# Optimization experiments

Measured on AMD Instinct MI355X. Metric: run time of the kernel, lower is better.

The kernel has to match this reference:

```python
import jax, jax.numpy as jnp
import numpy as np

G, N, DEG = 256, 128, 16          # graphs, nodes/graph, avg degree
C_IN, H, C_OUT = 128, 256, 128    # channels = [128,256,256,128]
K1, HEADS = 75, 4                 # GMT: ceil(0.25*300) seeds, 4 heads
NTOT, E = G * N, G * N * DEG
BN_EPS = 1e-5


def _bn(h, gamma, beta):
    # BatchNorm1d, training mode (biased batch stats over nodes)
    m = h.mean(0)
    v = h.var(0)
    return (h - m) * jax.lax.rsqrt(v + BN_EPS) * gamma + beta


def _gin(x, src, dst, W1, b1, g1, be1, W2, b2, g2, be2):
    # GINConv, eps=0: MLP(x + sum_{j->i} x_j); MLP = Lin-BN-ReLU-Lin-BN
    agg = x + jax.ops.segment_sum(x[src], dst, num_segments=NTOT)
    h = jax.nn.relu(_bn(agg @ W1 + b1, g1, be1))
    return _bn(h @ W2 + b2, g2, be2)


def _gcn(x, src, dst, W, b):
    # GCNConv with self-loops and symmetric normalization
    xw = x @ W
    deg = jax.ops.segment_sum(jnp.ones((E,), x.dtype), dst, num_segments=NTOT) + 1.0
    dinv = jax.lax.rsqrt(deg)
    msg = xw[src] * (dinv[src] * dinv[dst])[:, None]
    return jax.ops.segment_sum(msg, dst, num_segments=NTOT) + xw / deg[:, None] + b


def _mab(Q, Kd, Vd, Wq, bq, Wo, bo):
    # Multihead attention block of GMT (no layer_norm, no padding mask:
    # all graphs have exactly N nodes). O = Qp + MHA(Qp,K,V); out = O + relu(fc_o(O))
    Qp = Q @ Wq + bq                                   # [B, q, H]
    B, q, h = Qp.shape
    dh = h // HEADS
    sc = jnp.einsum('bqhd,bkhd->bhqk', Qp.reshape(B, q, HEADS, dh),
                    Kd.reshape(B, -1, HEADS, dh)) / jnp.sqrt(jnp.float32(h))
    A = jax.nn.softmax(sc, axis=-1)
    O = Qp + jnp.einsum('bhqk,bkhd->bqhd', A, Vd.reshape(B, -1, HEADS, dh)).reshape(B, q, h)
    return O + jax.nn.relu(O @ Wo + bo)


def _forward(x, edge_index, batch,
             g0_W1, g0_b1, g0_gamma1, g0_beta1, g0_W2, g0_b2, g0_gamma2, g0_beta2,
             g1_W1, g1_b1, g1_gamma1, g1_beta1, g1_W2, g1_b2, g1_gamma2, g1_beta2,
             lin1_W, lin1_b, S1,
             p1_Wq, p1_Wk, p1_Wv, p1_Wo, p1_bq, p1_bk, p1_bv, p1_bo,
             s2_Wq, s2_Wk, s2_Wv, s2_Wo, s2_bq, s2_bk, s2_bv, s2_bo,
             p3_Wq, p3_Wk, p3_Wv, p3_Wo, p3_bq, p3_bk, p3_bv, p3_bo,
             S3, lin2_W, lin2_b):
    src, dst = edge_index[0], edge_index[1]
    h = jax.nn.relu(_gin(x, src, dst, g0_W1, g0_b1, g0_gamma1, g0_beta1,
                         g0_W2, g0_b2, g0_gamma2, g0_beta2))
    h = jax.nn.relu(_gin(h, src, dst, g1_W1, g1_b1, g1_gamma1, g1_beta1,
                         g1_W2, g1_b2, g1_gamma2, g1_beta2))
    xl = h @ lin1_W + lin1_b                           # post-lin1 node feats [NTOT,H]
    # GMPool_G: PMA with K1 seeds, K/V from GCNConv over the graph
    Kd = _gcn(xl, src, dst, p1_Wk, p1_bk).reshape(G, N, H)
    Vd = _gcn(xl, src, dst, p1_Wv, p1_bv).reshape(G, N, H)
    Xp = _mab(jnp.broadcast_to(S1[None], (G, K1, H)), Kd, Vd, p1_Wq, p1_bq, p1_Wo, p1_bo)
    # SelfAtt: SAB
    Xp = _mab(Xp, Xp @ s2_Wk + s2_bk, Xp @ s2_Wv + s2_bv, s2_Wq, s2_bq, s2_Wo, s2_bo)
    # GMPool_I: PMA with 1 seed
    Xp = _mab(jnp.broadcast_to(S3[None], (G, 1, H)),
              Xp @ p3_Wk + p3_bk, Xp @ p3_Wv + p3_bv, p3_Wq, p3_bq, p3_Wo, p3_bo)
    return Xp[:, 0, :] @ lin2_W + lin2_b               # [G, C_OUT]


def setup_inputs() -> dict:
    key = jax.random.key(0)
    ks = iter(jax.random.split(key, 64))
    def p(shape, scale):
        return jax.random.normal(next(ks), shape, dtype=jnp.float32) * scale
    x = jax.random.normal(next(ks), (NTOT, C_IN), dtype=jnp.float32)
    src = jax.random.randint(next(ks), (G, N * DEG), 0, N, dtype=jnp.int32)
    dst = jax.random.randint(next(ks), (G, N * DEG), 0, N, dtype=jnp.int32)
    off = (jnp.arange(G, dtype=jnp.int32) * N)[:, None]
    edge_index = jnp.stack([(src + off).reshape(-1), (dst + off).reshape(-1)])
    batch = jnp.repeat(jnp.arange(G, dtype=jnp.int32), N)
    inp = {'x': x, 'edge_index': edge_index, 'batch': batch}
    for i, (ci, co) in enumerate([(C_IN, H), (H, H)]):
        inp[f'g{i}_W1'] = p((ci, co), ci ** -0.5)
        inp[f'g{i}_b1'] = jnp.zeros((co,), jnp.float32)
        inp[f'g{i}_gamma1'] = jnp.ones((co,), jnp.float32)
        inp[f'g{i}_beta1'] = jnp.zeros((co,), jnp.float32)
        inp[f'g{i}_W2'] = p((co, co), co ** -0.5)
        inp[f'g{i}_b2'] = jnp.zeros((co,), jnp.float32)
        inp[f'g{i}_gamma2'] = jnp.ones((co,), jnp.float32)
        inp[f'g{i}_beta2'] = jnp.zeros((co,), jnp.float32)
    inp['lin1_W'] = p((H, H), H ** -0.5)
    inp['lin1_b'] = jnp.zeros((H,), jnp.float32)
    inp['S1'] = p((K1, H), H ** -0.5)
    for pre in ['p1', 's2', 'p3']:
        for nm in ['Wq', 'Wk', 'Wv', 'Wo']:
            inp[f'{pre}_{nm}'] = p((H, H), H ** -0.5)
        for nm in ['bq', 'bk', 'bv', 'bo']:
            inp[f'{pre}_{nm}'] = jnp.zeros((H,), jnp.float32)
    inp['S3'] = p((1, H), H ** -0.5)
    inp['lin2_W'] = p((H, C_OUT), H ** -0.5)
    inp['lin2_b'] = jnp.zeros((C_OUT,), jnp.float32)
    return inp


def reference(x, edge_index, batch,
              g0_W1, g0_b1, g0_gamma1, g0_beta1, g0_W2, g0_b2, g0_gamma2, g0_beta2,
              g1_W1, g1_b1, g1_gamma1, g1_beta1, g1_W2, g1_b2, g1_gamma2, g1_beta2,
              lin1_W, lin1_b, S1,
              p1_Wq, p1_Wk, p1_Wv, p1_Wo, p1_bq, p1_bk, p1_bv, p1_bo,
              s2_Wq, s2_Wk, s2_Wv, s2_Wo, s2_bq, s2_bk, s2_bv, s2_bo,
              p3_Wq, p3_Wk, p3_Wv, p3_Wo, p3_bq, p3_bk, p3_bv, p3_bo,
              S3, lin2_W, lin2_b):
    return _forward(x, edge_index, batch,
                    g0_W1, g0_b1, g0_gamma1, g0_beta1, g0_W2, g0_b2, g0_gamma2, g0_beta2,
                    g1_W1, g1_b1, g1_gamma1, g1_beta1, g1_W2, g1_b2, g1_gamma2, g1_beta2,
                    lin1_W, lin1_b, S1,
                    p1_Wq, p1_Wk, p1_Wv, p1_Wo, p1_bq, p1_bk, p1_bv, p1_bo,
                    s2_Wq, s2_Wk, s2_Wv, s2_Wo, s2_bq, s2_bk, s2_bv, s2_bo,
                    p3_Wq, p3_Wk, p3_Wv, p3_Wo, p3_bq, p3_bk, p3_bv, p3_bo,
                    S3, lin2_W, lin2_b)
```

## Files before the change

### kernel.cpp

```cpp
#include <hip/hip_runtime.h>
#include <math.h>

#define GG 256
#define NN 128
#define NTOT (GG*NN)
#define EPG 2048
#define EDGES (GG*EPG)
#define HID 256
#define DH 64

typedef __attribute__((ext_vector_type(8))) short short8;
typedef __attribute__((ext_vector_type(4))) float f32x4;

__device__ __forceinline__ ushort f2bf(float f){
  union { float f; unsigned u; } x; x.f = f;
  unsigned r = x.u + 0x7fffu + ((x.u >> 16) & 1u);
  return (ushort)(r >> 16);
}
__device__ __forceinline__ float bf2f(ushort h){
  union { unsigned u; float f; } x; x.u = ((unsigned)h) << 16;
  return x.f;
}
__device__ __forceinline__ int permR(int p){
  return ((p>>2)&3)*16 + ((p>>4)&3)*4 + (p&3) + (p&64);
}

__global__ __launch_bounds__(256) void adj_build(
    const int* __restrict__ src, const int* __restrict__ dst,
    ushort* __restrict__ adjg, float* __restrict__ dinv)
{
  __shared__ unsigned hist[NN*NN];
  int g = blockIdx.x, t = threadIdx.x;
  int base = g*EPG, nb = g*NN;
  for (int i=t; i<NN*NN; i+=256) hist[i]=0u;
  __syncthreads();
  {
    int4 a = *(const int4*)(src + base + t*8);
    int4 b = *(const int4*)(src + base + t*8 + 4);
    int4 c = *(const int4*)(dst + base + t*8);
    int4 d = *(const int4*)(dst + base + t*8 + 4);
    atomicAdd(&hist[(a.x-nb)*NN + (c.x-nb)], 1u);
    atomicAdd(&hist[(a.y-nb)*NN + (c.y-nb)], 1u);
    atomicAdd(&hist[(a.z-nb)*NN + (c.z-nb)], 1u);
    atomicAdd(&hist[(a.w-nb)*NN + (c.w-nb)], 1u);
    atomicAdd(&hist[(b.x-nb)*NN + (d.x-nb)], 1u);
    atomicAdd(&hist[(b.y-nb)*NN + (d.y-nb)], 1u);
    atomicAdd(&hist[(b.z-nb)*NN + (d.z-nb)], 1u);
    atomicAdd(&hist[(b.w-nb)*NN + (d.w-nb)], 1u);
  }
  __syncthreads();
  if (t < NN){
    unsigned dg = 0;
    for (int k=0; k<NN; k++) dg += hist[k*NN + t];
    dinv[nb + t] = rsqrtf((float)dg + 1.0f);
  }
  __syncthreads();
  ushort* out = adjg + (size_t)g*NN*NN;
  for (int idx=t; idx<NN*NN; idx+=256){
    int i = idx >> 7, kp = idx & 127;
    int j = permR(kp);
    unsigned cnt = hist[j*NN + i];
    float v = (float)cnt + ((i==j) ? 1.0f : 0.0f);
    out[idx] = f2bf(v);
  }
}

template<int MODE, int OUTBF>
__global__ __launch_bounds__(256) void agg_gemm(
    const ushort* __restrict__ adjg,
    const ushort* __restrict__ P0, const ushort* __restrict__ P1,
    const float* __restrict__ aux,
    const float* __restrict__ b0, const float* __restrict__ b1,
    void* __restrict__ out0v, void* __restrict__ out1v,
    float* __restrict__ part)
{
  const int g = blockIdx.x;
  int bn, sel = 0;
  if (MODE==2){ sel = blockIdx.y >> 1; bn = (blockIdx.y & 1)*128; }
  else bn = blockIdx.y*128;
  const ushort* Ph = (MODE==2 && sel) ? P1 : P0;
  const float* bias = (MODE==2) ? (sel ? b1 : b0) : b0;
  void* outv = (MODE==2 && sel) ? out1v : out0v;
  const int t = threadIdx.x;
  const int w = t>>6, l = t&63;
  const int wr = w>>1, wc = w&1;
  const int c16 = l&15, g16 = l>>4;
  const size_t nbase = (size_t)g*NN;
  f32x4 acc[4][4];
  #pragma unroll
  for (int i=0;i<4;i++)
    #pragma unroll
    for (int j=0;j<4;j++) acc[i][j] = (f32x4){0.f,0.f,0.f,0.f};
  const ushort* ag = adjg + (size_t)g*NN*NN;

  float sclj[4], shfj[4];
  if (MODE==1){
    #pragma unroll
    for (int j=0;j<4;j++){
      int col = bn + wc*64 + j*16 + c16;
      sclj[j] = aux[col]; shfj[j] = aux[256+col];
    }
  }

  for (int kk=0; kk<128; kk+=32){
    short8 af[4];
    #pragma unroll
    for (int i=0;i<4;i++)
      af[i] = *(const short8*)(ag + (wr*64+i*16+c16)*NN + kk + g16*8);
    short8 bh[4];
    size_t off = nbase + kk + g16*8;
    #pragma unroll
    for (int j=0;j<4;j++){
      int col = bn + wc*64 + j*16 + c16;
      short8 h8 = *(const short8*)(Ph + (size_t)col*NTOT + off);
      if (MODE==1){
        #pragma unroll
        for (int e=0;e<8;e++){
          float v = bf2f((ushort)h8[e]);
          v = fmaxf(v*sclj[j] + shfj[j], 0.f);
          h8[e] = (short)f2bf(v);
        }
      }
      bh[j] = h8;
    }
    #pragma unroll
    for (int i=0;i<4;i++)
      #pragma unroll
      for (int j=0;j<4;j++)
        acc[i][j] = __builtin_amdgcn_mfma_f32_16x16x32_bf16(af[i], bh[j], acc[i][j], 0,0,0);
  }
  float sj[4]  = {0.f,0.f,0.f,0.f};
  float s2j[4] = {0.f,0.f,0.f,0.f};
  #pragma unroll
  for (int i=0;i<4;i++){
    float4 di4 = make_float4(1.f,1.f,1.f,1.f);
    if (MODE==2) di4 = *(const float4*)(aux + nbase + wr*64 + i*16 + g16*4);
    #pragma unroll
    for (int j=0;j<4;j++){
      int col = bn + wc*64 + j*16 + c16;
      #pragma unroll
      for (int r=0;r<4;r++){
        int row = wr*64 + i*16 + g16*4 + r;
        float v = acc[i][j][r];
        if (MODE==2) v = v*(&di4.x)[r] + bias[col];
        if (MODE==3){ v = v + (bias ? bias[col] : 0.f); sj[j]+=v; s2j[j]+=v*v; }
        if (OUTBF) ((ushort*)outv)[(nbase + row)*HID + col] = f2bf(v);
        else       ((float*)outv)[(nbase + row)*HID + col] = v;
      }
    }
  }
  if (MODE==3){
    #pragma unroll
    for (int j=0;j<4;j++){
      float s = sj[j], s2 = s2j[j];
      s  += __shfl_xor(s, 16);  s  += __shfl_xor(s, 32);
      s2 += __shfl_xor(s2,16);  s2 += __shfl_xor(s2,32);
      if (g16==0){
        int col = bn + wc*64 + j*16 + c16;
        part[(g*2+wr)*256 + col]          = s;
        part[131072 + (g*2+wr)*256 + col] = s2;
      }
    }
  }
}

struct PrepW { const float* w; int K; int N; };
struct PrepArgs { PrepW e[16]; };

__global__ __launch_bounds__(256) void prep_weights(PrepArgs pa, ushort* __restrict__ wtb)
{
  __shared__ ushort T[64][72];
  int wi = blockIdx.x;
  const float* W = pa.e[wi].w;
  int K = pa.e[wi].K, N = pa.e[wi].N;
  int tk_n = K>>6, tn_n = N>>6;
  int tile = blockIdx.y;
  if (tile >= tk_n*tn_n) return;
  int tk = tile % tk_n, tn = tile / tk_n;
  int t = threadIdx.x;
  int kr = t>>2, n0 = (t&3)*16;
  #pragma unroll
  for (int j=0;j<4;j++){
    float4 v = *(const float4*)(W + (size_t)(tk*64+kr)*N + tn*64 + n0 + j*4);
    T[n0+j*4+0][kr] = f2bf(v.x);
    T[n0+j*4+1][kr] = f2bf(v.y);
    T[n0+j*4+2][kr] = f2bf(v.z);
    T[n0+j*4+3][kr] = f2bf(v.w);
  }
  __syncthreads();
  ushort* out = wtb + (size_t)wi*65536;
  int nr = t>>2, k0 = (t&3)*16;
  *(short8*)(out + (size_t)(tn*64+nr)*K + tk*64 + k0)     = *(short8*)&T[nr][k0];
  *(short8*)(out + (size_t)(tn*64+nr)*K + tk*64 + k0 + 8) = *(short8*)&T[nr][k0+8];
}

__global__ __launch_bounds__(256) void comb_bias(
    const float* __restrict__ bl, const float* __restrict__ Wk,
    const float* __restrict__ Wv, float* __restrict__ bcomb)
{
  int n = threadIdx.x;
  const float* W = blockIdx.x ? Wv : Wk;
  float s = 0.f;
  for (int k=0;k<256;k++) s += bl[k]*W[k*256+n];
  bcomb[blockIdx.x*256+n] = s;
}

__global__ __launch_bounds__(256) void bnrelu_bf(
    const ushort* __restrict__ in, const float* __restrict__ stats,
    ushort* __restrict__ outp)
{
  size_t i = ((size_t)blockIdx.x*256 + threadIdx.x)*8;
  int c = (int)(i & 255);
  short8 h = *(const short8*)(in + i);
  float4 s0 = *(const float4*)(stats + c);
  float4 s1 = *(const float4*)(stats + c + 4);
  float4 h0 = *(const float4*)(stats + 256 + c);
  float4 h1 = *(const float4*)(stats + 256 + c + 4);
  float sc[8] = {s0.x,s0.y,s0.z,s0.w,s1.x,s1.y,s1.z,s1.w};
  float sh[8] = {h0.x,h0.y,h0.z,h0.w,h1.x,h1.y,h1.z,h1.w};
  #pragma unroll
  for (int e=0;e<8;e++){
    float v = fmaxf(bf2f((ushort)h[e])*sc[e] + sh[e], 0.f);
    h[e] = (short)f2bf(v);
  }
  *(short8*)(outp + i) = h;
}

__global__ __launch_bounds__(256) void bn_final2(const float* __restrict__ part,
    const float* __restrict__ gamma, const float* __restrict__ beta, float* __restrict__ stats)
{
  int c = blockIdx.x, t = threadIdx.x;
  float s  = part[(size_t)t*256+c]          + part[(size_t)(t+256)*256+c];
  float s2 = part[131072+(size_t)t*256+c]   + part[131072+(size_t)(t+256)*256+c];
  #pragma unroll
  for (int o=1;o<64;o<<=1){ s += __shfl_xor(s,o); s2 += __shfl_xor(s2,o); }
  __shared__ float ws[8];
  int wv = t>>6;
  if ((t&63)==0){ ws[wv]=s; ws[4+wv]=s2; }
  __syncthreads();
  if (t==0){
    float S  = ws[0]+ws[1]+ws[2]+ws[3];
    float S2 = ws[4]+ws[5]+ws[6]+ws[7];
    const float invn = 1.0f/(float)NTOT;
    float mean = S*invn;
    float var  = S2*invn - mean*mean;
    float scl  = gamma[c]*rsqrtf(var + 1e-5f);
    stats[c]     = scl;
    stats[256+c] = beta[c] - mean*scl;
  }
}

template<int EPI, int ATR, int BNF, int TW, int ABF, int OBF>
__global__ __launch_bounds__(256) void mm_bf16(
    const void* __restrict__ A, const ushort* __restrict__ Wt,
    const float* __restrict__ bias, const float* __restrict__ biasB,
    const float* __restrict__ biasC, const float* __restrict__ skip,
    const float* __restrict__ bnst,
    void* __restrict__ out, ushort* __restrict__ twp,
    const float* __restrict__ rscale, float* __restrict__ part,
    int M, int K, int N)
{
  __shared__ ushort Al[64][72];
  __shared__ ushort Bl[128][72];
  const int t = threadIdx.x;
  const int bm = blockIdx.x*64, bn = blockIdx.y*128;
  const int w = t>>6, l = t&63;
  const int c16 = l&15, g16 = l>>4;
  const int ar = t>>2, ac = (t&3)*16;
  const int br = t>>1, bc = (t&1)*32;
  f32x4 acc[4][2];
  #pragma unroll
  for (int i=0;i<4;i++)
    #pragma unroll
    for (int j=0;j<2;j++) acc[i][j] = (f32x4){0.f,0.f,0.f,0.f};

  for (int k0=0; k0<K; k0+=64){
    if (ABF){
      const ushort* apb = (const ushort*)A + (size_t)(bm+ar)*K + k0 + ac;
      short8 p0 = *(const short8*)apb;
      short8 p1 = *(const short8*)(apb + 8);
      if (ATR){
        int cb = k0 + ac;
        float scl[16], shf[16];
        *(float4*)&scl[0]  = *(const float4*)(bnst + cb);
        *(float4*)&scl[4]  = *(const float4*)(bnst + cb + 4);
        *(float4*)&scl[8]  = *(const float4*)(bnst + cb + 8);
        *(float4*)&scl[12] = *(const float4*)(bnst + cb + 12);
        *(float4*)&shf[0]  = *(const float4*)(bnst + 256 + cb);
        *(float4*)&shf[4]  = *(const float4*)(bnst + 256 + cb + 4);
        *(float4*)&shf[8]  = *(const float4*)(bnst + 256 + cb + 8);
        *(float4*)&shf[12] = *(const float4*)(bnst + 256 + cb + 12);
        #pragma unroll
        for (int e=0;e<8;e++){
          float v0 = bf2f((ushort)p0[e]);
          v0 = fmaxf(v0*scl[e] + shf[e], 0.f);
          p0[e] = (short)f2bf(v0);
          float v1 = bf2f((ushort)p1[e]);
          v1 = fmaxf(v1*scl[8+e] + shf[8+e], 0.f);
          p1[e] = (short)f2bf(v1);
        }
      }
      *(short8*)&Al[ar][ac]     = p0;
      *(short8*)&Al[ar][ac + 8] = p1;
    } else {
      const float* ap = (const float*)A + (size_t)(bm+ar)*K + k0 + ac;
      #pragma unroll
      for (int j=0;j<2;j++){
        float4 v0 = *(const float4*)(ap + j*8);
        float4 v1 = *(const float4*)(ap + j*8 + 4);
        if (ATR){
          int cb = k0 + ac + j*8;
          float4 s0 = *(const float4*)(bnst + cb);
          float4 s1 = *(const float4*)(bnst + cb + 4);
          float4 h0 = *(const float4*)(bnst + 256 + cb);
          float4 h1 = *(const float4*)(bnst + 256 + cb + 4);
          v0.x=fmaxf(v0.x*s0.x+h0.x,0.f); v0.y=fmaxf(v0.y*s0.y+h0.y,0.f);
          v0.z=fmaxf(v0.z*s0.z+h0.z,0.f); v0.w=fmaxf(v0.w*s0.w+h0.w,0.f);
          v1.x=fmaxf(v1.x*s1.x+h1.x,0.f); v1.y=fmaxf(v1.y*s1.y+h1.y,0.f);
          v1.z=fmaxf(v1.z*s1.z+h1.z,0.f); v1.w=fmaxf(v1.w*s1.w+h1.w,0.f);
        }
        short8 p;
        p[0]=(short)f2bf(v0.x); p[1]=(short)f2bf(v0.y); p[2]=(short)f2bf(v0.z); p[3]=(short)f2bf(v0.w);
        p[4]=(short)f2bf(v1.x); p[5]=(short)f2bf(v1.y); p[6]=(short)f2bf(v1.z); p[7]=(short)f2bf(v1.w);
        *(short8*)&Al[ar][ac+j*8] = p;
      }
    }
    const ushort* bp = Wt + (size_t)(bn+br)*K + k0 + bc;
    #pragma unroll
    for (int j=0;j<4;j++)
      *(short8*)&Bl[br][bc+j*8] = *(const short8*)(bp + j*8);
    __syncthreads();
    #pragma unroll
    for (int kk=0; kk<64; kk+=32){
      short8 af[4], bf[2];
      #pragma unroll
      for (int i=0;i<4;i++) af[i] = *(short8*)&Al[i*16+c16][kk+g16*8];
      #pragma unroll
      for (int j=0;j<2;j++) bf[j] = *(short8*)&Bl[w*32+j*16+c16][kk+g16*8];
      #pragma unroll
      for (int i=0;i<4;i++)
        #pragma unroll
        for (int j=0;j<2;j++)
          acc[i][j] = __builtin_amdgcn_mfma_f32_16x16x32_bf16(af[i], bf[j], acc[i][j], 0,0,0);
    }
    __syncthreads();
  }

  float sj[2]  = {0.f,0.f};
  float s2j[2] = {0.f,0.f};
  #pragma unroll
  for (int j=0;j<2;j++){
    const int col = bn + w*32 + j*16 + c16;
    const int seg = col >> 8;
    const float* bsel = (seg==0) ? bias : ((seg==1) ? biasB : biasC);
    const float bv = bsel ? bsel[col & 255] : 0.f;
    if (TW){
      short8 h8a, h8b;
      #pragma unroll
      for (int i=0;i<4;i++){
        float4 rs = make_float4(1.f,1.f,1.f,1.f);
        if (rscale) rs = *(const float4*)(rscale + bm + i*16 + g16*4);
        #pragma unroll
        for (int r=0;r<4;r++){
          float v = acc[i][j][r] + bv;
          if (BNF){ sj[j]+=v; s2j[j]+=v*v; }
          float sv = v * (&rs.x)[r];
          ushort hb = f2bf(sv);
          if (i<2) h8a[i*4+r]=(short)hb;
          else     h8b[(i-2)*4+r]=(short)hb;
        }
      }
      ushort* dst = twp + (size_t)col*NTOT + bm + g16*16;
      *(short8*)(dst)     = h8a;
      *(short8*)(dst + 8) = h8b;
    } else {
      #pragma unroll
      for (int i=0;i<4;i++){
        #pragma unroll
        for (int r=0;r<4;r++){
          int row = bm + i*16 + g16*4 + r;
          float v = acc[i][j][r] + bv;
          if (BNF){ sj[j]+=v; s2j[j]+=v*v; }
          if (EPI==1) v = skip[(size_t)row*N+col] + fmaxf(v,0.f);
          if (OBF) ((ushort*)out)[(size_t)row*N+col] = f2bf(v);
          else     ((float*)out)[(size_t)row*N+col] = v;
        }
      }
    }
  }
  if (BNF){
    #pragma unroll
    for (int j=0;j<2;j++){
      float s = sj[j], s2 = s2j[j];
      s  += __shfl_xor(s, 16);  s  += __shfl_xor(s, 32);
      s2 += __shfl_xor(s2,16);  s2 += __shfl_xor(s2,32);
      if (g16==0){
        int col = bn + w*32 + j*16 + c16;
        part[(bm>>6)*256 + col]          = s;
        part[131072 + (bm>>6)*256 + col] = s2;
      }
    }
  }
}

template<int EPI>
__global__ __launch_bounds__(256) void mm_kernel(
    const float* __restrict__ A, const float* __restrict__ W,
    const float* __restrict__ bias, const float* __restrict__ skip,
    float* __restrict__ out, int M, int K, int N)
{
  __shared__ float As[16][68];
  __shared__ float Ws[16][68];
  const int t  = threadIdx.x;
  const int bm = blockIdx.x*64, bn = blockIdx.y*64;
  const int tx = t & 15, ty = t >> 4;
  const int lrow = t >> 2;
  const int lkc  = (t & 3) * 4;
  const int wkr  = t >> 4;
  const int wnc  = (t & 15) * 4;
  float acc[4][4] = {{0.f}};
  for (int k0 = 0; k0 < K; k0 += 16) {
    float4 av = make_float4(0.f,0.f,0.f,0.f);
    if (bm + lrow < M) av = *(const float4*)(A + (size_t)(bm+lrow)*K + k0 + lkc);
    float4 wv = *(const float4*)(W + (size_t)(k0+wkr)*N + bn + wnc);
    As[lkc+0][lrow]=av.x; As[lkc+1][lrow]=av.y; As[lkc+2][lrow]=av.z; As[lkc+3][lrow]=av.w;
    *(float4*)&Ws[wkr][wnc] = wv;
    __syncthreads();
    #pragma unroll
    for (int kk=0; kk<16; kk++){
      float4 a4 = *(float4*)&As[kk][ty*4];
      float4 b4 = *(float4*)&Ws[kk][tx*4];
      acc[0][0]+=a4.x*b4.x; acc[0][1]+=a4.x*b4.y; acc[0][2]+=a4.x*b4.z; acc[0][3]+=a4.x*b4.w;
      acc[1][0]+=a4.y*b4.x; acc[1][1]+=a4.y*b4.y; acc[1][2]+=a4.y*b4.z; acc[1][3]+=a4.y*b4.w;
      acc[2][0]+=a4.z*b4.x; acc[2][1]+=a4.z*b4.y; acc[2][2]+=a4.z*b4.z; acc[2][3]+=a4.z*b4.w;
      acc[3][0]+=a4.w*b4.x; acc[3][1]+=a4.w*b4.y; acc[3][2]+=a4.w*b4.z; acc[3][3]+=a4.w*b4.w;
    }
    __syncthreads();
  }
  #pragma unroll
  for (int i=0;i<4;i++){
    int r = bm + ty*4 + i;
    if (r >= M) continue;
    #pragma unroll
    for (int j=0;j<4;j++){
      int c = bn + tx*4 + j;
      float v = acc[i][j] + (bias ? bias[c] : 0.f);
      if (EPI==1) v = skip[(size_t)r*N + c] + fmaxf(v, 0.f);
      out[(size_t)r*N + c] = v;
    }
  }
}

template<int KVBF, int QBF>
__global__ __launch_bounds__(256) void attn_mfma(
    const void* __restrict__ Qpv, const void* __restrict__ Kdv, const void* __restrict__ Vdv,
    float* __restrict__ O, int qlen, int klen, int qgstride, int qstride, int kvstride)
{
  __shared__ ushort Kbf[128*72];
  __shared__ ushort Vt[64*136];
  __shared__ ushort Pws[4][16*136];
  int g = blockIdx.x, h = blockIdx.y;
  int hd0 = h*DH;
  int t = threadIdx.x, w = t>>6, l = t&63;

  for (int idx=t; idx<128*16; idx+=256){
    int k = idx>>4, d4 = (idx&15)*4;
    ushort4 kb = make_ushort4(0,0,0,0), vb = kb;
    if (k < klen){
      if (KVBF){
        const ushort* Kd = (const ushort*)Kdv;
        const ushort* Vd = (const ushort*)Vdv;
        kb = *(const ushort4*)(Kd + ((size_t)g*klen + k)*kvstride + hd0 + d4);
        vb = *(const ushort4*)(Vd + ((size_t)g*klen + k)*kvstride + hd0 + d4);
      } else {
        const float* Kd = (const float*)Kdv;
        const float* Vd = (const float*)Vdv;
        float4 kv = *(const float4*)(Kd + ((size_t)g*klen + k)*kvstride + hd0 + d4);
        float4 vv = *(const float4*)(Vd + ((size_t)g*klen + k)*kvstride + hd0 + d4);
        kb = make_ushort4(f2bf(kv.x), f2bf(kv.y), f2bf(kv.z), f2bf(kv.w));
        vb = make_ushort4(f2bf(vv.x), f2bf(vv.y), f2bf(vv.z), f2bf(vv.w));
      }
    }
    *(ushort4*)&Kbf[k*72 + d4] = kb;
    Vt[(d4+0)*136 + k] = vb.x;
    Vt[(d4+1)*136 + k] = vb.y;
    Vt[(d4+2)*136 + k] = vb.z;
    Vt[(d4+3)*136 + k] = vb.w;
  }
  __syncthreads();

  const int c16 = l & 15, g16 = l >> 4;
  const float scl = 1.0f/16.0f;
  int qtiles = (qlen + 15) >> 4;
  for (int qt = w; qt < qtiles; qt += 4){
    int qbase = qt*16;
    int qrow = qbase + c16; if (qrow > qlen-1) qrow = qlen-1;
    short8 qa[2];
    if (QBF){
      const ushort* qr = (const ushort*)Qpv + (size_t)g*qgstride + (size_t)qrow*qstride + hd0 + g16*8;
      qa[0] = *(const short8*)(qr);
      qa[1] = *(const short8*)(qr + 32);
    } else {
      const float* qr = (const float*)Qpv + (size_t)g*qgstride + (size_t)qrow*qstride + hd0 + g16*8;
      #pragma unroll
      for (int dh=0; dh<2; dh++){
        float4 x0 = *(const float4*)(qr + dh*32);
        float4 x1 = *(const float4*)(qr + dh*32 + 4);
        short8 f;
        f[0]=(short)f2bf(x0.x); f[1]=(short)f2bf(x0.y); f[2]=(short)f2bf(x0.z); f[3]=(short)f2bf(x0.w);
        f[4]=(short)f2bf(x1.x); f[5]=(short)f2bf(x1.y); f[6]=(short)f2bf(x1.z); f[7]=(short)f2bf(x1.w);
        qa[dh]=f;
      }
    }
    float p[8][4];
    #pragma unroll
    for (int kt=0; kt<8; kt++){
      f32x4 a = {0.f,0.f,0.f,0.f};
      short8 b0 = *(short8*)&Kbf[(kt*16+c16)*72 + g16*8];
      short8 b1 = *(short8*)&Kbf[(kt*16+c16)*72 + 32 + g16*8];
      a = __builtin_amdgcn_mfma_f32_16x16x32_bf16(qa[0], b0, a, 0,0,0);
      a = __builtin_amdgcn_mfma_f32_16x16x32_bf16(qa[1], b1, a, 0,0,0);
      int k = kt*16 + c16;
      #pragma unroll
      for (int r=0; r<4; r++) p[kt][r] = (k < klen) ? a[r]*scl : -1e30f;
    }
    float m[4], sum[4];
    #pragma unroll
    for (int r=0; r<4; r++){
      float mm = p[0][r];
      #pragma unroll
      for (int kt=1; kt<8; kt++) mm = fmaxf(mm, p[kt][r]);
      for (int o=1; o<16; o<<=1) mm = fmaxf(mm, __shfl_xor(mm, o));
      m[r] = mm;
    }
    #pragma unroll
    for (int r=0; r<4; r++){
      float s = 0.f;
      #pragma unroll
      for (int kt=0; kt<8; kt++){ p[kt][r] = __expf(p[kt][r]-m[r]); s += p[kt][r]; }
      for (int o=1; o<16; o<<=1) s += __shfl_xor(s, o);
      sum[r] = 1.0f/s;
    }
    #pragma unroll
    for (int kt=0; kt<8; kt++)
      #pragma unroll
      for (int r=0; r<4; r++)
        Pws[w][(g16*4+r)*136 + kt*16 + c16] = f2bf(p[kt][r]*sum[r]);
    #pragma unroll
    for (int dt=0; dt<4; dt++){
      f32x4 o4 = {0.f,0.f,0.f,0.f};
      #pragma unroll
      for (int ks=0; ks<4; ks++){
        short8 pa = *(short8*)&Pws[w][c16*136 + ks*32 + g16*8];
        short8 vb = *(short8*)&Vt[(dt*16+c16)*136 + ks*32 + g16*8];
        o4 = __builtin_amdgcn_mfma_f32_16x16x32_bf16(pa, vb, o4, 0,0,0);
      }
      #pragma unroll
      for (int r=0; r<4; r++){
        int q2 = qbase + g16*4 + r;
        if (q2 < qlen){
          int col = hd0 + dt*16 + c16;
          float qv;
          if (QBF) qv = bf2f(((const ushort*)Qpv)[(size_t)g*qgstride + (size_t)q2*qstride + col]);
          else     qv = ((const float*)Qpv)[(size_t)g*qgstride + (size_t)q2*qstride + col];
          O[((size_t)g*qlen + q2)*HID + col] = qv + o4[r];
        }
      }
    }
  }
}

extern "C" void kernel_launch(void* const* d_in, const int* in_sizes, int n_in,
                              void* d_out, int out_size, void* d_ws, size_t ws_size,
                              hipStream_t stream)
{
  (void)in_sizes; (void)n_in; (void)out_size; (void)ws_size;
  const float* x      = (const float*)d_in[0];
  const int*   ei     = (const int*)d_in[1];
  const float* g0_W1=(const float*)d_in[3],  *g0_b1=(const float*)d_in[4],  *g0_ga1=(const float*)d_in[5],  *g0_be1=(const float*)d_in[6];
  const float* g0_W2=(const float*)d_in[7],  *g0_b2=(const float*)d_in[8],  *g0_ga2=(const float*)d_in[9],  *g0_be2=(const float*)d_in[10];
  const float* g1_W1=(const float*)d_in[11], *g1_b1=(const float*)d_in[12], *g1_ga1=(const float*)d_in[13], *g1_be1=(const float*)d_in[14];
  const float* g1_W2=(const float*)d_in[15], *g1_b2=(const float*)d_in[16], *g1_ga2=(const float*)d_in[17], *g1_be2=(const float*)d_in[18];
  const float* lin1_W=(const float*)d_in[19], *lin1_b=(const float*)d_in[20];
  const float* S1=(const float*)d_in[21];
  const float* p1_Wq=(const float*)d_in[22], *p1_Wk=(const float*)d_in[23], *p1_Wv=(const float*)d_in[24], *p1_Wo=(const float*)d_in[25];
  const float* p1_bq=(const float*)d_in[26], *p1_bk=(const float*)d_in[27], *p1_bv=(const float*)d_in[28], *p1_bo=(const float*)d_in[29];
  const float* s2_Wq=(const float*)d_in[30], *s2_Wk=(const float*)d_in[31], *s2_Wv=(const float*)d_in[32], *s2_Wo=(const float*)d_in[33];
  const float* s2_bq=(const float*)d_in[34], *s2_bk=(const float*)d_in[35], *s2_bv=(const float*)d_in[36], *s2_bo=(const float*)d_in[37];
  const float* p3_Wq=(const float*)d_in[38], *p3_Wk=(const float*)d_in[39], *p3_Wv=(const float*)d_in[40], *p3_Wo=(const float*)d_in[41];
  const float* p3_bq=(const float*)d_in[42], *p3_bk=(const float*)d_in[43], *p3_bv=(const float*)d_in[44], *p3_bo=(const float*)d_in[45];
  const float* S3=(const float*)d_in[46];
  const float* lin2_W=(const float*)d_in[47], *lin2_b=(const float*)d_in[48];

  const int* src = ei;
  const int* dst = ei + EDGES;

  float* F = (float*)d_ws;
  const size_t SZ = (size_t)NTOT*HID;
  float* R0=F, *R1=F+SZ, *R2=F+2*SZ, *R3=F+3*SZ;
  float* part  = F + 4*SZ;
  float* stats = part + 262144;
  float* dinv  = stats + 512;
  float* qp1   = dinv + 32768;
  float* qp3   = qp1 + 19200;
  float* bcomb = qp3 + 256;
  float* o3    = bcomb + 512;
  float* xf    = o3 + 65536;
  ushort* adjg = (ushort*)(xf + 65536);
  ushort* wtb  = adjg + (size_t)GG*NN*NN;

  const dim3 B256(256);
  const dim3 mmBig(512,2), mmMid(300,2);
  #define WT(i) (wtb + (size_t)(i)*65536)

  PrepArgs pa;
  pa.e[0]  = {g0_W1, 128, 256};
  pa.e[1]  = {g0_W2, 256, 256};
  pa.e[2]  = {g1_W1, 256, 256};
  pa.e[3]  = {g1_W2, 256, 256};
  pa.e[4]  = {lin1_W,256, 256};
  pa.e[5]  = {p1_Wk, 256, 256};
  pa.e[6]  = {p1_Wv, 256, 256};
  pa.e[7]  = {p1_Wo, 256, 256};
  pa.e[8]  = {s2_Wk, 256, 256};
  pa.e[9]  = {s2_Wv, 256, 256};
  pa.e[10] = {s2_Wq, 256, 256};
  pa.e[11] = {s2_Wo, 256, 256};
  pa.e[12] = {p3_Wk, 256, 256};
  pa.e[13] = {p3_Wv, 256, 256};
  pa.e[14] = {p3_Wo, 256, 256};
  pa.e[15] = {lin2_W,256, 128};
  prep_weights<<<dim3(16,16),B256,0,stream>>>(pa, wtb);

  {
    float* tmpK = part;
    float* tmpV = part + 65536;
    mm_kernel<0><<<dim3(4,4),B256,0,stream>>>(lin1_W, p1_Wk, nullptr, nullptr, tmpK, 256,256,256);
    mm_kernel<0><<<dim3(4,4),B256,0,stream>>>(lin1_W, p1_Wv, nullptr, nullptr, tmpV, 256,256,256);
    comb_bias<<<dim3(2),B256,0,stream>>>(lin1_b, p1_Wk, p1_Wv, bcomb);
    PrepArgs pc;
    pc.e[0] = {tmpK, 256, 256};
    pc.e[1] = {tmpV, 256, 256};
    prep_weights<<<dim3(2,16),B256,0,stream>>>(pc, WT(5));
  }

  adj_build<<<GG,B256,0,stream>>>(src,dst,adjg,dinv);

  mm_bf16<0,0,0,1,0,0><<<mmBig,B256,0,stream>>>(x, WT(0), nullptr,nullptr,nullptr, nullptr, nullptr, nullptr, (ushort*)R1, nullptr, nullptr, NTOT,128,HID);
  agg_gemm<3,1><<<dim3(GG,2),B256,0,stream>>>(adjg, (ushort*)R1, nullptr, nullptr, g0_b1, nullptr, R0, nullptr, part);
  bn_final2<<<dim3(256),B256,0,stream>>>(part, g0_ga1, g0_be1, stats);
  bnrelu_bf<<<dim3(4096),B256,0,stream>>>((ushort*)R0, stats, (ushort*)R3);
  mm_bf16<0,0,1,1,1,0><<<mmBig,B256,0,stream>>>(R3, WT(1), g0_b2, nullptr,nullptr, nullptr, nullptr, nullptr, (ushort*)R2, nullptr, part, NTOT,256,HID);
  bn_final2<<<dim3(256),B256,0,stream>>>(part, g0_ga2, g0_be2, stats);

  agg_gemm<1,1><<<dim3(GG,2),B256,0,stream>>>(adjg, (ushort*)R2, nullptr, stats, nullptr, nullptr, R0, nullptr, nullptr);
  mm_bf16<0,0,1,0,1,1><<<mmBig,B256,0,stream>>>(R0, WT(2), g1_b1, nullptr,nullptr, nullptr, nullptr, R1, nullptr, nullptr, part, NTOT,256,HID);
  bn_final2<<<dim3(256),B256,0,stream>>>(part, g1_ga1, g1_be1, stats);
  bnrelu_bf<<<dim3(4096),B256,0,stream>>>((ushort*)R1, stats, (ushort*)R3);
  mm_bf16<0,0,1,0,1,1><<<mmBig,B256,0,stream>>>(R3, WT(3), g1_b2, nullptr,nullptr, nullptr, nullptr, R2, nullptr, nullptr, part, NTOT,256,HID);
  bn_final2<<<dim3(256),B256,0,stream>>>(part, g1_ga2, g1_be2, stats);

  bnrelu_bf<<<dim3(4096),B256,0,stream>>>((ushort*)R2, stats, (ushort*)R1);

  mm_bf16<0,0,0,1,1,0><<<dim3(512,4),B256,0,stream>>>(R1, WT(5), bcomb, bcomb+256, nullptr, nullptr, nullptr, nullptr, (ushort*)R0, dinv, nullptr, NTOT,256,512);
  {
    void* Kb = (void*)R3;
    void* Vb = (void*)((ushort*)R3 + (size_t)NTOT*HID);
    agg_gemm<2,1><<<dim3(GG,4),B256,0,stream>>>(adjg, (ushort*)R0, (ushort*)R0 + (size_t)256*NTOT, dinv, p1_bk, p1_bv, Kb, Vb, nullptr);
    mm_kernel<0><<<dim3(2,4),B256,0,stream>>>(S1, p1_Wq, p1_bq, nullptr, qp1, 75,256,HID);
    attn_mfma<1,0><<<dim3(GG,4),B256,0,stream>>>(qp1, Kb, Vb, R2, 75,128, 0, HID, HID);
  }
  mm_bf16<1,0,0,0,0,1><<<mmMid,B256,0,stream>>>(R2, WT(7), p1_bo, nullptr,nullptr, R2, nullptr, R1, nullptr, nullptr, nullptr, 19200,256,HID);

  {
    ushort* KVQ = (ushort*)R0;
    mm_bf16<0,0,0,0,1,1><<<dim3(300,6),B256,0,stream>>>(R1, WT(8), s2_bk, s2_bv, s2_bq, nullptr, nullptr, KVQ, nullptr, nullptr, nullptr, 19200,256,768);
    attn_mfma<1,1><<<dim3(GG,4),B256,0,stream>>>((const void*)(KVQ+512), (const void*)KVQ, (const void*)(KVQ+256), R3, 75,75, 75*768, 768, 768);
  }
  mm_bf16<1,0,0,0,0,1><<<mmMid,B256,0,stream>>>(R3, WT(11), s2_bo, nullptr,nullptr, R3, nullptr, R1, nullptr, nullptr, nullptr, 19200,256,HID);

  {
    ushort* KV3 = (ushort*)R2;
    mm_bf16<0,0,0,0,1,1><<<dim3(300,4),B256,0,stream>>>(R1, WT(12), p3_bk, p3_bv, nullptr, nullptr, nullptr, KV3, nullptr, nullptr, nullptr, 19200,256,512);
    mm_kernel<0><<<dim3(1,4),B256,0,stream>>>(S3, p3_Wq, p3_bq, nullptr, qp3, 1,256,HID);
    attn_mfma<1,0><<<dim3(GG,4),B256,0,stream>>>(qp3, (const void*)KV3, (const void*)(KV3+256), o3, 1,75, 0, HID, 512);
  }
  mm_bf16<1,0,0,0,0,0><<<dim3(4,2),B256,0,stream>>>(o3, WT(14), p3_bo, nullptr,nullptr, o3, nullptr, xf, nullptr, nullptr, nullptr, 256,256,HID);

  mm_bf16<0,0,0,0,0,0><<<dim3(4,1),B256,0,stream>>>(xf, WT(15), lin2_b, nullptr,nullptr, nullptr, nullptr, (float*)d_out, nullptr, nullptr, nullptr, 256,256,128);
}
```

Baseline: 400.9 us.

## Merge weight prep, adjacency build and small projections into one fused prep kernel

Replaces several small independent launches (weight bf16 transposes, adjacency histogram build, the lin1·Wk/Wv products, combined bias, and the S1/S3 query projections) with one kernel whose block ranges dispatch to each job. This cuts launch overhead and lets these tiny jobs run concurrently instead of back to back. The fused kernel reserves 64KB of shared memory for every block, which limits occupancy for the light jobs. The mm_bf16 shared tiles are also padded from 72 to 76 columns to change the LDS bank pattern.

```diff
diff --git a/kernel.cpp b/kernel.cpp
--- a/kernel.cpp
+++ b/kernel.cpp
@@ -25,44 +25,158 @@
   return ((p>>2)&3)*16 + ((p>>4)&3)*4 + (p&3) + (p&64);
 }
 
-__global__ __launch_bounds__(256) void adj_build(
+struct PrepW { const float* w; int K; int N; };
+struct PrepArgs { PrepW e[16]; };
+
+__device__ __forceinline__ void prepw_body(char* smem, const float* W, int K, int N,
+                                           ushort* out, int tk, int tn)
+{
+  ushort (*T)[72] = (ushort (*)[72])smem;
+  int t = threadIdx.x;
+  int kr = t>>2, n0 = (t&3)*16;
+  #pragma unroll
+  for (int j=0;j<4;j++){
+    float4 v = *(const float4*)(W + (size_t)(tk*64+kr)*N + tn*64 + n0 + j*4);
+    T[n0+j*4+0][kr] = f2bf(v.x);
+    T[n0+j*4+1][kr] = f2bf(v.y);
+    T[n0+j*4+2][kr] = f2bf(v.z);
+    T[n0+j*4+3][kr] = f2bf(v.w);
+  }
+  __syncthreads();
+  int nr = t>>2, k0 = (t&3)*16;
+  *(short8*)(out + (size_t)(tn*64+nr)*K + tk*64 + k0)     = *(short8*)&T[nr][k0];
+  *(short8*)(out + (size_t)(tn*64+nr)*K + tk*64 + k0 + 8) = *(short8*)&T[nr][k0+8];
+}
+
+__device__ __forceinline__ void mmk_body(char* smem, const float* A, const float* W,
+    const float* bias, float* out, int bm, int bn, int M, int K, int N)
+{
+  float (*As)[68] = (float (*)[68])smem;
+  float (*Ws)[68] = (float (*)[68])(smem + 16*68*4);
+  const int t  = threadIdx.x;
+  const int tx = t & 15, ty = t >> 4;
+  const int lrow = t >> 2;
+  const int lkc  = (t & 3) * 4;
+  const int wkr  = t >> 4;
+  const int wnc  = (t & 15) * 4;
+  float acc[4][4] = {{0.f}};
+  for (int k0 = 0; k0 < K; k0 += 16) {
+    float4 av = make_float4(0.f,0.f,0.f,0.f);
+    if (bm + lrow < M) av = *(const float4*)(A + (size_t)(bm+lrow)*K + k0 + lkc);
+    float4 wv = *(const float4*)(W + (size_t)(k0+wkr)*N + bn + wnc);
+    As[lkc+0][lrow]=av.x; As[lkc+1][lrow]=av.y; As[lkc+2][lrow]=av.z; As[lkc+3][lrow]=av.w;
+    *(float4*)&Ws[wkr][wnc] = wv;
+    __syncthreads();
+    #pragma unroll
+    for (int kk=0; kk<16; kk++){
+      float4 a4 = *(float4*)&As[kk][ty*4];
+      float4 b4 = *(float4*)&Ws[kk][tx*4];
+      acc[0][0]+=a4.x*b4.x; acc[0][1]+=a4.x*b4.y; acc[0][2]+=a4.x*b4.z; acc[0][3]+=a4.x*b4.w;
+      acc[1][0]+=a4.y*b4.x; acc[1][1]+=a4.y*b4.y; acc[1][2]+=a4.y*b4.z; acc[1][3]+=a4.y*b4.w;
+      acc[2][0]+=a4.z*b4.x; acc[2][1]+=a4.z*b4.y; acc[2][2]+=a4.z*b4.z; acc[2][3]+=a4.z*b4.w;
+      acc[3][0]+=a4.w*b4.x; acc[3][1]+=a4.w*b4.y; acc[3][2]+=a4.w*b4.z; acc[3][3]+=a4.w*b4.w;
+    }
+    __syncthreads();
+  }
+  #pragma unroll
+  for (int i=0;i<4;i++){
+    int r = bm + ty*4 + i;
+    if (r >= M) continue;
+    #pragma unroll
+    for (int j=0;j<4;j++){
+      int c = bn + tx*4 + j;
+      float v = acc[i][j] + (bias ? bias[c] : 0.f);
+      out[(size_t)r*N + c] = v;
+    }
+  }
+}
+
+__global__ __launch_bounds__(256) void fat_prep(
+    PrepArgs pa, ushort* __restrict__ wtb,
     const int* __restrict__ src, const int* __restrict__ dst,
-    ushort* __restrict__ adjg, float* __restrict__ dinv)
-{
-  __shared__ unsigned hist[NN*NN];
-  int g = blockIdx.x, t = threadIdx.x;
-  int base = g*EPG, nb = g*NN;
-  for (int i=t; i<NN*NN; i+=256) hist[i]=0u;
-  __syncthreads();
-  {
-    int4 a = *(const int4*)(src + base + t*8);
-    int4 b = *(const int4*)(src + base + t*8 + 4);
-    int4 c = *(const int4*)(dst + base + t*8);
-    int4 d = *(const int4*)(dst + base + t*8 + 4);
-    atomicAdd(&hist[(a.x-nb)*NN + (c.x-nb)], 1u);
-    atomicAdd(&hist[(a.y-nb)*NN + (c.y-nb)], 1u);
-    atomicAdd(&hist[(a.z-nb)*NN + (c.z-nb)], 1u);
-    atomicAdd(&hist[(a.w-nb)*NN + (c.w-nb)], 1u);
-    atomicAdd(&hist[(b.x-nb)*NN + (d.x-nb)], 1u);
-    atomicAdd(&hist[(b.y-nb)*NN + (d.y-nb)], 1u);
-    atomicAdd(&hist[(b.z-nb)*NN + (d.z-nb)], 1u);
-    atomicAdd(&hist[(b.w-nb)*NN + (d.w-nb)], 1u);
-  }
-  __syncthreads();
-  if (t < NN){
-    unsigned dg = 0;
-    for (int k=0; k<NN; k++) dg += hist[k*NN + t];
-    dinv[nb + t] = rsqrtf((float)dg + 1.0f);
-  }
-  __syncthreads();
-  ushort* out = adjg + (size_t)g*NN*NN;
-  for (int idx=t; idx<NN*NN; idx+=256){
-    int i = idx >> 7, kp = idx & 127;
-    int j = permR(kp);
-    unsigned cnt = hist[j*NN + i];
-    float v = (float)cnt + ((i==j) ? 1.0f : 0.0f);
-    out[idx] = f2bf(v);
-  }
+    ushort* __restrict__ adjg, float* __restrict__ dinv,
+    const float* lin1_W, const float* p1_Wk, const float* p1_Wv,
+    const float* lin1_b, float* bcomb, float* tmpK, float* tmpV,
+    const float* S1, const float* p1_Wq, const float* p1_bq, float* qp1,
+    const float* S3, const float* p3_Wq, const float* p3_bq, float* qp3)
+{
+  __shared__ char smem[65536];
+  const int b = blockIdx.x;
+  const int t = threadIdx.x;
+
+  if (b < 256){
+    int wi = b>>4, tile = b&15;
+    const float* W = pa.e[wi].w;
+    int K = pa.e[wi].K, N = pa.e[wi].N;
+    int tk_n = K>>6, tn_n = N>>6;
+    if (tile >= tk_n*tn_n) return;
+    prepw_body(smem, W, K, N, wtb + (size_t)wi*65536, tile % tk_n, tile / tk_n);
+  } else if (b < 512){
+    int g = b - 256;
+    unsigned* hist = (unsigned*)smem;
+    int base = g*EPG, nb = g*NN;
+    for (int i=t; i<NN*NN; i+=256) hist[i]=0u;
+    __syncthreads();
+    {
+      int4 a = *(const int4*)(src + base + t*8);
+      int4 bb = *(const int4*)(src + base + t*8 + 4);
+      int4 c = *(const int4*)(dst + base + t*8);
+      int4 d = *(const int4*)(dst + base + t*8 + 4);
+      atomicAdd(&hist[(a.x-nb)*NN + (c.x-nb)], 1u);
+      atomicAdd(&hist[(a.y-nb)*NN + (c.y-nb)], 1u);
+      atomicAdd(&hist[(a.z-nb)*NN + (c.z-nb)], 1u);
+      atomicAdd(&hist[(a.w-nb)*NN + (c.w-nb)], 1u);
+      atomicAdd(&hist[(bb.x-nb)*NN + (d.x-nb)], 1u);
+      atomicAdd(&hist[(bb.y-nb)*NN + (d.y-nb)], 1u);
+      atomicAdd(&hist[(bb.z-nb)*NN + (d.z-nb)], 1u);
+      atomicAdd(&hist[(bb.w-nb)*NN + (d.w-nb)], 1u);
+    }
+    __syncthreads();
+    if (t < NN){
+      unsigned dg = 0;
+      for (int k=0; k<NN; k++) dg += hist[k*NN + t];
+      dinv[nb + t] = rsqrtf((float)dg + 1.0f);
+    }
+    __syncthreads();
+    ushort* out = adjg + (size_t)g*NN*NN;
+    for (int idx=t; idx<NN*NN; idx+=256){
+      int i = idx >> 7, kp = idx & 127;
+      int j = permR(kp);
+      unsigned cnt = hist[j*NN + i];
+      float v = (float)cnt + ((i==j) ? 1.0f : 0.0f);
+      out[idx] = f2bf(v);
+    }
+  } else if (b < 528){
+    int idx = b - 512;
+    mmk_body(smem, lin1_W, p1_Wk, nullptr, tmpK, (idx&3)*64, (idx>>2)*64, 256,256,256);
+  } else if (b < 544){
+    int idx = b - 528;
+    mmk_body(smem, lin1_W, p1_Wv, nullptr, tmpV, (idx&3)*64, (idx>>2)*64, 256,256,256);
+  } else if (b < 546){
+    int sel = b - 544;
+    const float* W = sel ? p1_Wv : p1_Wk;
+    float s = 0.f;
+    for (int k=0;k<256;k++) s += lin1_b[k]*W[k*256+t];
+    bcomb[sel*256+t] = s;
+  } else if (b < 554){
+    int idx = b - 546;
+    mmk_body(smem, S1, p1_Wq, p1_bq, qp1, (idx&1)*64, (idx>>1)*64, 75,256,HID);
+  } else {
+    int idx = b - 554;
+    mmk_body(smem, S3, p3_Wq, p3_bq, qp3, 0, idx*64, 1,256,HID);
+  }
+}
+
+__global__ __launch_bounds__(256) void prep_weights(PrepArgs pa, ushort* __restrict__ wtb)
+{
+  __shared__ char smem[9216];
+  int wi = blockIdx.x;
+  const float* W = pa.e[wi].w;
+  int K = pa.e[wi].K, N = pa.e[wi].N;
+  int tk_n = K>>6, tn_n = N>>6;
+  int tile = blockIdx.y;
+  if (tile >= tk_n*tn_n) return;
+  prepw_body(smem, W, K, N, wtb + (size_t)wi*65536, tile % tk_n, tile / tk_n);
 }
 
 template<int MODE, int OUTBF>
@@ -162,47 +276,6 @@
       }
     }
   }
-}
-
-struct PrepW { const float* w; int K; int N; };
-struct PrepArgs { PrepW e[16]; };
-
-__global__ __launch_bounds__(256) void prep_weights(PrepArgs pa, ushort* __restrict__ wtb)
-{
-  __shared__ ushort T[64][72];
-  int wi = blockIdx.x;
-  const float* W = pa.e[wi].w;
-  int K = pa.e[wi].K, N = pa.e[wi].N;
-  int tk_n = K>>6, tn_n = N>>6;
-  int tile = blockIdx.y;
-  if (tile >= tk_n*tn_n) return;
-  int tk = tile % tk_n, tn = tile / tk_n;
-  int t = threadIdx.x;
-  int kr = t>>2, n0 = (t&3)*16;
-  #pragma unroll
-  for (int j=0;j<4;j++){
-    float4 v = *(const float4*)(W + (size_t)(tk*64+kr)*N + tn*64 + n0 + j*4);
-    T[n0+j*4+0][kr] = f2bf(v.x);
-    T[n0+j*4+1][kr] = f2bf(v.y);
-    T[n0+j*4+2][kr] = f2bf(v.z);
-    T[n0+j*4+3][kr] = f2bf(v.w);
-  }
-  __syncthreads();
-  ushort* out = wtb + (size_t)wi*65536;
-  int nr = t>>2, k0 = (t&3)*16;
-  *(short8*)(out + (size_t)(tn*64+nr)*K + tk*64 + k0)     = *(short8*)&T[nr][k0];
-  *(short8*)(out + (size_t)(tn*64+nr)*K + tk*64 + k0 + 8) = *(short8*)&T[nr][k0+8];
-}
-
-__global__ __launch_bounds__(256) void comb_bias(
-    const float* __restrict__ bl, const float* __restrict__ Wk,
-    const float* __restrict__ Wv, float* __restrict__ bcomb)
-{
-  int n = threadIdx.x;
-  const float* W = blockIdx.x ? Wv : Wk;
-  float s = 0.f;
-  for (int k=0;k<256;k++) s += bl[k]*W[k*256+n];
-  bcomb[blockIdx.x*256+n] = s;
 }
 
 __global__ __launch_bounds__(256) void bnrelu_bf(
@@ -260,8 +333,8 @@
     const float* __restrict__ rscale, float* __restrict__ part,
     int M, int K, int N)
 {
-  __shared__ ushort Al[64][72];
-  __shared__ ushort Bl[128][72];
+  __shared__ ushort Al[64][76];
+  __shared__ ushort Bl[128][76];
   const int t = threadIdx.x;
   const int bm = blockIdx.x*64, bn = blockIdx.y*128;
   const int w = t>>6, l = t&63;
@@ -403,54 +476,6 @@
   }
 }
 
-template<int EPI>
-__global__ __launch_bounds__(256) void mm_kernel(
-    const float* __restrict__ A, const float* __restrict__ W,
-    const float* __restrict__ bias, const float* __restrict__ skip,
-    float* __restrict__ out, int M, int K, int N)
-{
-  __shared__ float As[16][68];
-  __shared__ float Ws[16][68];
-  const int t  = threadIdx.x;
-  const int bm = blockIdx.x*64, bn = blockIdx.y*64;
-  const int tx = t & 15, ty = t >> 4;
-  const int lrow = t >> 2;
-  const int lkc  = (t & 3) * 4;
-  const int wkr  = t >> 4;
-  const int wnc  = (t & 15) * 4;
-  float acc[4][4] = {{0.f}};
-  for (int k0 = 0; k0 < K; k0 += 16) {
-    float4 av = make_float4(0.f,0.f,0.f,0.f);
-    if (bm + lrow < M) av = *(const float4*)(A + (size_t)(bm+lrow)*K + k0 + lkc);
-    float4 wv = *(const float4*)(W + (size_t)(k0+wkr)*N + bn + wnc);
-    As[lkc+0][lrow]=av.x; As[lkc+1][lrow]=av.y; As[lkc+2][lrow]=av.z; As[lkc+3][lrow]=av.w;
-    *(float4*)&Ws[wkr][wnc] = wv;
-    __syncthreads();
-    #pragma unroll
-    for (int kk=0; kk<16; kk++){
-      float4 a4 = *(float4*)&As[kk][ty*4];
-      float4 b4 = *(float4*)&Ws[kk][tx*4];
-      acc[0][0]+=a4.x*b4.x; acc[0][1]+=a4.x*b4.y; acc[0][2]+=a4.x*b4.z; acc[0][3]+=a4.x*b4.w;
-      acc[1][0]+=a4.y*b4.x; acc[1][1]+=a4.y*b4.y; acc[1][2]+=a4.y*b4.z; acc[1][3]+=a4.y*b4.w;
-      acc[2][0]+=a4.z*b4.x; acc[2][1]+=a4.z*b4.y; acc[2][2]+=a4.z*b4.z; acc[2][3]+=a4.z*b4.w;
-      acc[3][0]+=a4.w*b4.x; acc[3][1]+=a4.w*b4.y; acc[3][2]+=a4.w*b4.z; acc[3][3]+=a4.w*b4.w;
-    }
-    __syncthreads();
-  }
-  #pragma unroll
-  for (int i=0;i<4;i++){
-    int r = bm + ty*4 + i;
-    if (r >= M) continue;
-    #pragma unroll
-    for (int j=0;j<4;j++){
-      int c = bn + tx*4 + j;
-      float v = acc[i][j] + (bias ? bias[c] : 0.f);
-      if (EPI==1) v = skip[(size_t)r*N + c] + fmaxf(v, 0.f);
-      out[(size_t)r*N + c] = v;
-    }
-  }
-}
-
 template<int KVBF, int QBF>
 __global__ __launch_bounds__(256) void attn_mfma(
     const void* __restrict__ Qpv, const void* __restrict__ Kdv, const void* __restrict__ Vdv,
@@ -606,7 +631,8 @@
   float* bcomb = qp3 + 256;
   float* o3    = bcomb + 512;
   float* xf    = o3 + 65536;
-  ushort* adjg = (ushort*)(xf + 65536);
+  float* tmpKV = xf + 65536;
+  ushort* adjg = (ushort*)(tmpKV + 131072);
   ushort* wtb  = adjg + (size_t)GG*NN*NN;
 
   const dim3 B256(256);
@@ -630,21 +656,17 @@
   pa.e[13] = {p3_Wv, 256, 256};
   pa.e[14] = {p3_Wo, 256, 256};
   pa.e[15] = {lin2_W,256, 128};
-  prep_weights<<<dim3(16,16),B256,0,stream>>>(pa, wtb);
-
+  float* tmpK = tmpKV;
+  float* tmpV = tmpKV + 65536;
+  fat_prep<<<dim3(558),B256,0,stream>>>(pa, wtb, src, dst, adjg, dinv,
+      lin1_W, p1_Wk, p1_Wv, lin1_b, bcomb, tmpK, tmpV,
+      S1, p1_Wq, p1_bq, qp1, S3, p3_Wq, p3_bq, qp3);
   {
-    float* tmpK = part;
-    float* tmpV = part + 65536;
-    mm_kernel<0><<<dim3(4,4),B256,0,stream>>>(lin1_W, p1_Wk, nullptr, nullptr, tmpK, 256,256,256);
-    mm_kernel<0><<<dim3(4,4),B256,0,stream>>>(lin1_W, p1_Wv, nullptr, nullptr, tmpV, 256,256,256);
-    comb_bias<<<dim3(2),B256,0,stream>>>(lin1_b, p1_Wk, p1_Wv, bcomb);
     PrepArgs pc;
     pc.e[0] = {tmpK, 256, 256};
     pc.e[1] = {tmpV, 256, 256};
     prep_weights<<<dim3(2,16),B256,0,stream>>>(pc, WT(5));
   }
-
-  adj_build<<<GG,B256,0,stream>>>(src,dst,adjg,dinv);
 
   mm_bf16<0,0,0,1,0,0><<<mmBig,B256,0,stream>>>(x, WT(0), nullptr,nullptr,nullptr, nullptr, nullptr, nullptr, (ushort*)R1, nullptr, nullptr, NTOT,128,HID);
   agg_gemm<3,1><<<dim3(GG,2),B256,0,stream>>>(adjg, (ushort*)R1, nullptr, nullptr, g0_b1, nullptr, R0, nullptr, part);
@@ -667,7 +689,6 @@
     void* Kb = (void*)R3;
     void* Vb = (void*)((ushort*)R3 + (size_t)NTOT*HID);
     agg_gemm<2,1><<<dim3(GG,4),B256,0,stream>>>(adjg, (ushort*)R0, (ushort*)R0 + (size_t)256*NTOT, dinv, p1_bk, p1_bv, Kb, Vb, nullptr);
-    mm_kernel<0><<<dim3(2,4),B256,0,stream>>>(S1, p1_Wq, p1_bq, nullptr, qp1, 75,256,HID);
     attn_mfma<1,0><<<dim3(GG,4),B256,0,stream>>>(qp1, Kb, Vb, R2, 75,128, 0, HID, HID);
   }
   mm_bf16<1,0,0,0,0,1><<<mmMid,B256,0,stream>>>(R2, WT(7), p1_bo, nullptr,nullptr, R2, nullptr, R1, nullptr, nullptr, nullptr, 19200,256,HID);
@@ -682,7 +703,6 @@
   {
     ushort* KV3 = (ushort*)R2;
     mm_bf16<0,0,0,0,1,1><<<dim3(300,4),B256,0,stream>>>(R1, WT(12), p3_bk, p3_bv, nullptr, nullptr, nullptr, KV3, nullptr, nullptr, nullptr, 19200,256,512);
-    mm_kernel<0><<<dim3(1,4),B256,0,stream>>>(S3, p3_Wq, p3_bq, nullptr, qp3, 1,256,HID);
     attn_mfma<1,0><<<dim3(GG,4),B256,0,stream>>>(qp3, (const void*)KV3, (const void*)(KV3+256), o3, 1,75, 0, HID, 512);
   }
   mm_bf16<1,0,0,0,0,0><<<dim3(4,2),B256,0,stream>>>(o3, WT(14), p3_bo, nullptr,nullptr, o3, nullptr, xf, nullptr, nullptr, nullptr, 256,256,HID);
```

New measurement: 343.1 us. 14.4% less time.
